# Optimization experiments

Measured on AMD Instinct MI355X. Metric: run time of the kernel, lower is better.

## Reference

```python
import jax, jax.numpy as jnp
import numpy as np

ROPE_BASE = 100.0


def _rope1d(tok, pos):
    # tok: [B, H, N, d], pos: [B, N] int. Matches croco apply_rope1d.
    d = tok.shape[-1]
    inv_freq = 1.0 / (ROPE_BASE ** (jnp.arange(0, d, 2, dtype=jnp.float32) / d))  # [d/2]
    ang = pos[:, None, :, None].astype(jnp.float32) * inv_freq  # [B,1,N,d/2]
    ang = jnp.concatenate([ang, ang], axis=-1)  # [B,1,N,d]
    cos, sin = jnp.cos(ang).astype(tok.dtype), jnp.sin(ang).astype(tok.dtype)
    x1, x2 = tok[..., : d // 2], tok[..., d // 2 :]
    rot = jnp.concatenate([-x2, x1], axis=-1)  # rotate_half
    return tok * cos + rot * sin


def _rope2d(tok, pos):
    # tok: [B, H, N, D]; first half of D uses pos[...,0] (y), second half pos[...,1] (x)
    y, x = jnp.split(tok, 2, axis=-1)
    return jnp.concatenate([_rope1d(y, pos[..., 0]), _rope1d(x, pos[..., 1])], axis=-1)


def setup_inputs() -> dict:
    key = jax.random.key(0)
    ks = jax.random.split(key, 10)
    B, N, C = 8, 1024, 768
    s = 0.02
    return {
        "query": jax.random.normal(ks[0], (B, N, C), jnp.float32),
        "key": jax.random.normal(ks[1], (B, N, C), jnp.float32),
        "value": jax.random.normal(ks[2], (B, N, C), jnp.float32),
        "qpos": jax.random.randint(ks[3], (B, N, 2), 0, 32, jnp.int32),
        "kpos": jax.random.randint(ks[4], (B, N, 2), 0, 32, jnp.int32),
        "Wq": jax.random.normal(ks[5], (C, C), jnp.float32) * s,
        "Wk": jax.random.normal(ks[6], (C, C), jnp.float32) * s,
        "Wv": jax.random.normal(ks[7], (C, C), jnp.float32) * s,
        "Wo": jax.random.normal(ks[8], (C, C), jnp.float32) * s,
        "bo": jnp.zeros((C,), jnp.float32),
    }


def reference(query, key, value, qpos, kpos, Wq, Wk, Wv, Wo, bo):
    B, Nq, C = query.shape
    H = 12
    hd = C // H
    scale = hd ** -0.5
    # projections (torch Linear: x @ W^T), then split heads -> [B,H,N,hd]
    q = jnp.einsum("bnc,dc->bnd", query, Wq).reshape(B, Nq, H, hd).transpose(0, 2, 1, 3)
    k = jnp.einsum("bnc,dc->bnd", key, Wk).reshape(B, -1, H, hd).transpose(0, 2, 1, 3)
    v = jnp.einsum("bnc,dc->bnd", value, Wv).reshape(B, -1, H, hd).transpose(0, 2, 1, 3)
    q = _rope2d(q, qpos)
    k = _rope2d(k, kpos)
    attn = jnp.einsum("bhqd,bhkd->bhqk", q, k) * scale
    attn = jax.nn.softmax(attn, axis=-1)
    x = jnp.einsum("bhqk,bhkd->bhqd", attn, v)
    x = x.transpose(0, 2, 1, 3).reshape(B, Nq, C)
    return jnp.einsum("bnc,dc->bnd", x, Wo) + bo
```

## Files before the change

kernel.cpp:

```cpp
#include <hip/hip_runtime.h>
#include <hip/hip_bf16.h>
#include <hip/hip_fp16.h>

#define B_DIM 8
#define N_DIM 1024
#define C_DIM 768
#define H_DIM 12
#define HD    64
#define M_DIM (B_DIM * N_DIM)
#define BH    (B_DIM * H_DIM)

static constexpr size_t TEN = (size_t)M_DIM * C_DIM;
static constexpr size_t WN  = (size_t)C_DIM * C_DIM;

typedef __attribute__((ext_vector_type(8))) short    s16x8;
typedef __attribute__((ext_vector_type(8))) _Float16 f16x8;
typedef __attribute__((ext_vector_type(4))) float    f32x4;

__device__ __forceinline__ unsigned short f2h(float f) {
    __half h = __float2half(f);
    return __half_as_ushort(h);
}


__global__ __launch_bounds__(256)
void convX(const float* __restrict__ q, const float* __restrict__ k,
           const float* __restrict__ v, unsigned short* __restrict__ XS)
{
    const int t  = blockIdx.z;
    const int p  = blockIdx.y;
    const int kb = blockIdx.x;
    const float* src = (t == 0) ? q : (t == 1 ? k : v);
    unsigned short* dst = XS + (size_t)t * TEN;

    const int mr = threadIdx.x & 127;
    const int gh = threadIdx.x >> 7;
    const float* s = src + ((size_t)(p * 128 + mr)) * C_DIM + kb * 32 + gh * 16;
    float4 v0 = *(const float4*)(s);
    float4 v1 = *(const float4*)(s + 4);
    float4 v2 = *(const float4*)(s + 8);
    float4 v3 = *(const float4*)(s + 12);
    float f[16] = {v0.x,v0.y,v0.z,v0.w, v1.x,v1.y,v1.z,v1.w,
                   v2.x,v2.y,v2.z,v2.w, v3.x,v3.y,v3.z,v3.w};
    #pragma unroll
    for (int gj = 0; gj < 2; ++gj) {
        int gg = gh * 2 + gj;
        s16x8 h8;
        #pragma unroll
        for (int e = 0; e < 8; ++e)
            h8[e] = (short)f2h(f[gj * 8 + e]);
        size_t a = ((((size_t)p * 24 + kb) * 4 + gg) * 128 + mr) * 8;
        *(s16x8*)(dst + a) = h8;
    }
}

__global__ __launch_bounds__(256)
void convW(const float* __restrict__ wq, const float* __restrict__ wk,
           const float* __restrict__ wv, const float* __restrict__ wo,
           unsigned short* __restrict__ WS)
{
    const int t  = blockIdx.z;
    const int p  = blockIdx.y;
    const int kb = blockIdx.x;
    const float* src = (t == 0) ? wq : (t == 1 ? wk : (t == 2 ? wv : wo));
    unsigned short* dst = WS + (size_t)t * WN;

    const int mr = threadIdx.x & 127;
    const int gh = threadIdx.x >> 7;
    const float* s = src + ((size_t)(p * 128 + mr)) * C_DIM + kb * 32 + gh * 16;
    float4 v0 = *(const float4*)(s);
    float4 v1 = *(const float4*)(s + 4);
    float4 v2 = *(const float4*)(s + 8);
    float4 v3 = *(const float4*)(s + 12);
    float f[16] = {v0.x,v0.y,v0.z,v0.w, v1.x,v1.y,v1.z,v1.w,
                   v2.x,v2.y,v2.z,v2.w, v3.x,v3.y,v3.z,v3.w};
    #pragma unroll
    for (int gj = 0; gj < 2; ++gj) {
        int gg = gh * 2 + gj;
        s16x8 h8;
        #pragma unroll
        for (int e = 0; e < 8; ++e)
            h8[e] = (short)f2h(f[gj * 8 + e]);
        size_t a = ((((size_t)p * 24 + kb) * 4 + gg) * 128 + mr) * 8;
        *(s16x8*)(dst + a) = h8;
    }
}

__global__ void angles512(float2* __restrict__ tab)
{
    int t = threadIdx.x;
    int pos = t >> 4, j = t & 15;
    float ang = (float)pos * exp2f(-(float)j * 0.41524101186092029f);
    float s, c;
    sincosf(ang, &s, &c);
    tab[t] = make_float2(c, s);
}

template<int MODE>
__global__ __launch_bounds__(256)
void gemmF(const unsigned short* __restrict__ XQ, const unsigned short* __restrict__ XK,
           const unsigned short* __restrict__ XV,
           const unsigned short* __restrict__ WQ, const unsigned short* __restrict__ WK,
           const unsigned short* __restrict__ WV,
           const int* __restrict__ qpos, const int* __restrict__ kpos,
           const float2* __restrict__ tab,
           unsigned short* __restrict__ OQ, unsigned short* __restrict__ OK_,
           unsigned short* __restrict__ OV,
           const float* __restrict__ bias, float* __restrict__ Of)
{
    __shared__ unsigned short sA[2][4][128][8];
    __shared__ unsigned short sB[2][4][128][8];

    const int tid  = threadIdx.x;
    const int lane = tid & 63;
    const int w    = tid >> 6;
    const int wr   = w >> 1, wc = w & 1;
    const int c    = lane & 15, g = lane >> 4;

    const int chunk = gridDim.x >> 3;
    const int wgid  = (blockIdx.x & 7) * chunk + (blockIdx.x >> 3);
    int z, m0, n0;
    if (MODE == 1) {
        z = wgid / 384;
        int r = wgid - z * 384;
        m0 = (r / 6) * 128;
        n0 = (r % 6) * 128;
    } else {
        z = 0;
        m0 = (wgid / 6) * 128;
        n0 = (wgid % 6) * 128;
    }

    const unsigned short *Ap, *Bp;
    if (MODE == 0 || z == 0) { Ap = XQ; Bp = WQ; }
    else if (z == 1)         { Ap = XK; Bp = WK; }
    else                     { Ap = XV; Bp = WV; }

    const size_t abase0 = (size_t)(m0 >> 7) * 24 * 4096;
    const size_t bbase0 = (size_t)(n0 >> 7) * 24 * 4096;

    f32x4 acc[4][4] = {};

    auto stage = [&](int kb, int buf) {
        #pragma unroll
        for (int t = 0; t < 4; ++t) {
            int is = w * 4 + t;
            int sel = is >> 3;
            int j   = is & 7;
            int gg  = j >> 1, half = j & 1;
            const unsigned short* srcp =
                (sel ? Bp + bbase0 : Ap + abase0) + (size_t)kb * 4096
                + (size_t)gg * 1024 + (half * 64 + lane) * 8;
            unsigned short* dstp = sel ? &sB[buf][gg][half * 64][0]
                                       : &sA[buf][gg][half * 64][0];
            __builtin_amdgcn_global_load_lds(
                (const __attribute__((address_space(1))) void*)srcp,
                (__attribute__((address_space(3))) void*)dstp,
                16, 0, 0);
        }
    };

    stage(0, 0);
    stage(1, 1);

    for (int kb = 0; kb < 24; ++kb) {
        int buf = kb & 1;
        if (kb < 23) asm volatile("s_waitcnt vmcnt(4)" ::: "memory");
        else         asm volatile("s_waitcnt vmcnt(0)" ::: "memory");
        __builtin_amdgcn_sched_barrier(0);
        __builtin_amdgcn_s_barrier();
        __builtin_amdgcn_sched_barrier(0);

        f16x8 a[4], b[4];
        #pragma unroll
        for (int mi = 0; mi < 4; ++mi)
            a[mi] = *(const f16x8*)&sA[buf][g][wr * 64 + 16 * mi + c][0];
        #pragma unroll
        for (int ni = 0; ni < 4; ++ni)
            b[ni] = *(const f16x8*)&sB[buf][g][wc * 64 + 16 * ni + c][0];
        __builtin_amdgcn_s_setprio(1);
        #pragma unroll
        for (int mi = 0; mi < 4; ++mi)
            #pragma unroll
            for (int ni = 0; ni < 4; ++ni)
                acc[mi][ni] = __builtin_amdgcn_mfma_f32_16x16x32_f16(a[mi], b[ni], acc[mi][ni], 0, 0, 0);
        __builtin_amdgcn_s_setprio(0);

        __builtin_amdgcn_sched_barrier(0);
        __builtin_amdgcn_s_barrier();
        __builtin_amdgcn_sched_barrier(0);
        if (kb + 2 < 24) stage(kb + 2, buf);
    }

    if (MODE == 0) {
        #pragma unroll
        for (int ni = 0; ni < 4; ++ni) {
            int d = n0 + wc * 64 + 16 * ni + c;
            float bv = bias[d];
            #pragma unroll
            for (int mi = 0; mi < 4; ++mi)
                #pragma unroll
                for (int r = 0; r < 4; ++r) {
                    int m = m0 + wr * 64 + 16 * mi + 4 * g + r;
                    Of[(size_t)m * C_DIM + d] = acc[mi][ni][r] + bv;
                }
        }
    } else if (z == 2) {
        #pragma unroll
        for (int ni = 0; ni < 4; ++ni) {
            int d = n0 + wc * 64 + 16 * ni + c;
            #pragma unroll
            for (int mi = 0; mi < 4; ++mi)
                #pragma unroll
                for (int r = 0; r < 4; ++r) {
                    int m = m0 + wr * 64 + 16 * mi + 4 * g + r;
                    OV[(size_t)m * C_DIM + d] = f2h(acc[mi][ni][r]);
                }
        }
    } else {
        const int* P = z ? kpos : qpos;
        unsigned short* T = z ? OK_ : OQ;
        const float scale = z ? 1.0f : 0.18033688011112042f;
        const int hh = (n0 >> 6) + wc;
        #pragma unroll
        for (int mi = 0; mi < 4; ++mi)
            #pragma unroll
            for (int r = 0; r < 4; ++r) {
                int m = m0 + wr * 64 + 16 * mi + 4 * g + r;
                int b = m >> 10, n = m & 1023;
                size_t base = ((size_t)(b * H_DIM + hh) * N_DIM + n) * HD;
                #pragma unroll
                for (int bb = 0; bb < 2; ++bb) {
                    int pos = P[2 * m + bb];
                    float2 cs = tab[pos * 16 + c];
                    float x1 = acc[mi][bb * 2 + 0][r];
                    float x2 = acc[mi][bb * 2 + 1][r];
                    float r1 = (x1 * cs.x - x2 * cs.y) * scale;
                    float r2 = (x2 * cs.x + x1 * cs.y) * scale;
                    T[base + bb * 32 + c]      = f2h(r1);
                    T[base + bb * 32 + 16 + c] = f2h(r2);
                }
            }
    }
}

__global__ __launch_bounds__(256)
void vtrans(const unsigned short* __restrict__ Vf, unsigned short* __restrict__ Vt)
{
    __shared__ unsigned short T[64][72];
    const int bh = blockIdx.y;
    const int nt = blockIdx.x;
    const int tid = threadIdx.x;
    const int b = bh / H_DIM, h = bh % H_DIM;
    const size_t hb = (size_t)bh * (N_DIM * HD);

    #pragma unroll
    for (int it = 0; it < 2; ++it) {
        int f = tid + it * 256;
        int r = f >> 3;
        int c8 = (f & 7) * 8;
        s16x8 v = *(const s16x8*)(Vf + ((size_t)(b * N_DIM + nt * 64 + r)) * C_DIM + h * HD + c8);
        #pragma unroll
        for (int j = 0; j < 8; ++j)
            T[c8 + j][r] = (unsigned short)v[j];
    }
    __syncthreads();
    #pragma unroll
    for (int it = 0; it < 2; ++it) {
        int f = tid + it * 256;
        int d = f >> 3;
        int nn = (f & 7) * 8;
        *(s16x8*)(Vt + hb + (size_t)d * N_DIM + nt * 64 + nn) = *(const s16x8*)&T[d][nn];
    }
}

__global__ __launch_bounds__(256)
void attn_f16(const unsigned short* __restrict__ Qh, const unsigned short* __restrict__ Kh,
              const unsigned short* __restrict__ Vt,
              unsigned short* __restrict__ Xb)
{
    __shared__ _Float16 sK[64][72];
    __shared__ _Float16 sV[64][72];
    __shared__ _Float16 sP[4][2][16][72];

    const int tid  = threadIdx.x;
    const int lane = tid & 63;
    const int wv   = tid >> 6;
    const int c    = lane & 15;
    const int g    = lane >> 4;

    const int bid   = blockIdx.x;
    const int xcd   = bid & 7;
    const int local = bid >> 3;
    const int bh    = xcd * 12 + (local >> 3);
    const int q0    = (local & 7) * 128;
    const size_t hb = (size_t)bh * (N_DIM * HD);

    const size_t qoffA = hb + (size_t)(q0 + wv * 32 + c) * HD;
    const size_t qoffB = qoffA + (size_t)16 * HD;
    f16x8 qA0 = *(const f16x8*)(Qh + qoffA + 8 * g);
    f16x8 qA1 = *(const f16x8*)(Qh + qoffA + 32 + 8 * g);
    f16x8 qB0 = *(const f16x8*)(Qh + qoffB + 8 * g);
    f16x8 qB1 = *(const f16x8*)(Qh + qoffB + 32 + 8 * g);

    f16x8 ones;
    #pragma unroll
    for (int e = 0; e < 8; ++e) ones[e] = (_Float16)1.0f;

    f32x4 accA[4] = {}, accB[4] = {};
    f32x4 lAcc[2] = {};

    for (int kt = 0; kt < 16; ++kt) {
        __syncthreads();
        #pragma unroll
        for (int it = 0; it < 2; ++it) {
            int f = tid + it * 256;
            int row = f >> 3;
            int ch = (f & 7) * 8;
            *(s16x8*)&sK[row][ch] = *(const s16x8*)(Kh + hb + (size_t)(kt * 64 + row) * HD + ch);
            *(s16x8*)&sV[row][ch] = *(const s16x8*)(Vt + hb + (size_t)row * N_DIM + kt * 64 + ch);
        }
        __syncthreads();

        f32x4 sA[4] = {}, sB[4] = {};
        __builtin_amdgcn_s_setprio(1);
        #pragma unroll
        for (int st = 0; st < 4; ++st) {
            f16x8 a0 = *(const f16x8*)&sK[16 * st + c][8 * g];
            f16x8 a1 = *(const f16x8*)&sK[16 * st + c][32 + 8 * g];
            sA[st] = __builtin_amdgcn_mfma_f32_16x16x32_f16(a0, qA0, sA[st], 0, 0, 0);
            sA[st] = __builtin_amdgcn_mfma_f32_16x16x32_f16(a1, qA1, sA[st], 0, 0, 0);
            sB[st] = __builtin_amdgcn_mfma_f32_16x16x32_f16(a0, qB0, sB[st], 0, 0, 0);
            sB[st] = __builtin_amdgcn_mfma_f32_16x16x32_f16(a1, qB1, sB[st], 0, 0, 0);
        }
        __builtin_amdgcn_s_setprio(0);

        #pragma unroll
        for (int st = 0; st < 4; ++st) {
            float pA[4], pB[4];
            #pragma unroll
            for (int r = 0; r < 4; ++r) {
                pA[r] = __builtin_amdgcn_exp2f(sA[st][r]);
                pB[r] = __builtin_amdgcn_exp2f(sB[st][r]);
            }
            __half2 a01 = __float22half2_rn(make_float2(pA[0], pA[1]));
            __half2 a23 = __float22half2_rn(make_float2(pA[2], pA[3]));
            __half2 b01 = __float22half2_rn(make_float2(pB[0], pB[1]));
            __half2 b23 = __float22half2_rn(make_float2(pB[2], pB[3]));
            *(uint2*)&sP[wv][0][c][16 * st + 4 * g] =
                make_uint2(*(unsigned*)&a01, *(unsigned*)&a23);
            *(uint2*)&sP[wv][1][c][16 * st + 4 * g] =
                make_uint2(*(unsigned*)&b01, *(unsigned*)&b23);
        }

        __builtin_amdgcn_s_setprio(1);
        #pragma unroll
        for (int m = 0; m < 2; ++m) {
            f16x8 pbA = *(const f16x8*)&sP[wv][0][c][32 * m + 8 * g];
            f16x8 pbB = *(const f16x8*)&sP[wv][1][c][32 * m + 8 * g];
            #pragma unroll
            for (int sd = 0; sd < 4; ++sd) {
                f16x8 va = *(const f16x8*)&sV[16 * sd + c][32 * m + 8 * g];
                accA[sd] = __builtin_amdgcn_mfma_f32_16x16x32_f16(va, pbA, accA[sd], 0, 0, 0);
                accB[sd] = __builtin_amdgcn_mfma_f32_16x16x32_f16(va, pbB, accB[sd], 0, 0, 0);
            }
            lAcc[0] = __builtin_amdgcn_mfma_f32_16x16x32_f16(ones, pbA, lAcc[0], 0, 0, 0);
            lAcc[1] = __builtin_amdgcn_mfma_f32_16x16x32_f16(ones, pbB, lAcc[1], 0, 0, 0);
        }
        __builtin_amdgcn_s_setprio(0);
    }

    float invA = 1.0f / lAcc[0][0];
    float invB = 1.0f / lAcc[1][0];

    const int b = bh / H_DIM, h = bh % H_DIM;
    #pragma unroll
    for (int sub = 0; sub < 2; ++sub) {
        const f32x4* acc = sub ? accB : accA;
        float invl = sub ? invB : invA;
        const int q = q0 + wv * 32 + sub * 16 + c;
        const int m  = b * N_DIM + q;
        const int p_ = m >> 7, mr = m & 127;
        #pragma unroll
        for (int sd = 0; sd < 4; ++sd) {
            int kdim = h * 64 + 16 * sd + 4 * g;
            int kb = kdim >> 5;
            int gg = (kdim >> 3) & 3;
            int e  = kdim & 7;
            size_t a = ((((size_t)p_ * 24 + kb) * 4 + gg) * 128 + mr) * 8 + e;
            unsigned short hs[4];
            #pragma unroll
            for (int r = 0; r < 4; ++r)
                hs[r] = f2h(acc[sd][r] * invl);
            *(uint2*)(Xb + a) =
                make_uint2((unsigned)hs[0] | ((unsigned)hs[1] << 16),
                           (unsigned)hs[2] | ((unsigned)hs[3] << 16));
        }
    }
}

extern "C" void kernel_launch(void* const* d_in, const int* in_sizes, int n_in,
                              void* d_out, int out_size, void* d_ws, size_t ws_size,
                              hipStream_t stream)
{
    const float* query = (const float*)d_in[0];
    const float* key_  = (const float*)d_in[1];
    const float* value = (const float*)d_in[2];
    const int*   qpos  = (const int*)d_in[3];
    const int*   kpos  = (const int*)d_in[4];
    const float* Wq    = (const float*)d_in[5];
    const float* Wk    = (const float*)d_in[6];
    const float* Wv    = (const float*)d_in[7];
    const float* Wo    = (const float*)d_in[8];
    const float* bo    = (const float*)d_in[9];
    float* out = (float*)d_out;

    unsigned short* XS  = (unsigned short*)d_ws;
    unsigned short* WS  = XS + 3 * TEN;
    unsigned short* Qh  = WS + 4 * WN;
    unsigned short* Kh  = Qh + TEN;
    unsigned short* Vf  = Kh + TEN;
    unsigned short* Vt  = Vf + TEN;
    unsigned short* Xb  = Vt + TEN;
    float2* tab = (float2*)(Xb + TEN);

    angles512<<<1, 512, 0, stream>>>(tab);
    convX<<<dim3(24, 64, 3), 256, 0, stream>>>(query, key_, value, XS);
    convW<<<dim3(24, 6, 4), 256, 0, stream>>>(Wq, Wk, Wv, Wo, WS);

    gemmF<1><<<dim3(1152), 256, 0, stream>>>(
        XS + 0 * TEN, XS + 1 * TEN, XS + 2 * TEN,
        WS + 0 * WN, WS + 1 * WN, WS + 2 * WN,
        qpos, kpos, tab, Qh, Kh, Vf, nullptr, nullptr);

    vtrans<<<dim3(N_DIM / 64, BH), 256, 0, stream>>>(Vf, Vt);

    attn_f16<<<dim3(768), 256, 0, stream>>>(Qh, Kh, Vt, Xb);

    gemmF<0><<<dim3(384), 256, 0, stream>>>(
        Xb, nullptr, nullptr,
        WS + 3 * WN, nullptr, nullptr,
        nullptr, nullptr, nullptr, nullptr, nullptr, nullptr, bo, out);
}
```

Before: 144.7 us.

## Triple-buffer GEMM LDS staging and register-prefetch K/V tiles in attention

```diff
diff --git a/kernel.cpp b/kernel.cpp
--- a/kernel.cpp
+++ b/kernel.cpp
@@ -108,8 +108,8 @@
            unsigned short* __restrict__ OV,
            const float* __restrict__ bias, float* __restrict__ Of)
 {
-    __shared__ unsigned short sA[2][4][128][8];
-    __shared__ unsigned short sB[2][4][128][8];
+    __shared__ unsigned short sA[3][4][128][8];
+    __shared__ unsigned short sB[3][4][128][8];
 
     const int tid  = threadIdx.x;
     const int lane = tid & 63;
@@ -162,11 +162,13 @@
 
     stage(0, 0);
     stage(1, 1);
+    stage(2, 2);
 
     for (int kb = 0; kb < 24; ++kb) {
-        int buf = kb & 1;
-        if (kb < 23) asm volatile("s_waitcnt vmcnt(4)" ::: "memory");
-        else         asm volatile("s_waitcnt vmcnt(0)" ::: "memory");
+        int buf = kb % 3;
+        if (kb < 22)      asm volatile("s_waitcnt vmcnt(8)" ::: "memory");
+        else if (kb == 22) asm volatile("s_waitcnt vmcnt(4)" ::: "memory");
+        else               asm volatile("s_waitcnt vmcnt(0)" ::: "memory");
         __builtin_amdgcn_sched_barrier(0);
         __builtin_amdgcn_s_barrier();
         __builtin_amdgcn_sched_barrier(0);
@@ -189,7 +191,7 @@
         __builtin_amdgcn_sched_barrier(0);
         __builtin_amdgcn_s_barrier();
         __builtin_amdgcn_sched_barrier(0);
-        if (kb + 2 < 24) stage(kb + 2, buf);
+        if (kb + 3 < 24) stage(kb + 3, buf);
     }
 
     if (MODE == 0) {
@@ -310,17 +312,36 @@
     f32x4 accA[4] = {}, accB[4] = {};
     f32x4 lAcc[2] = {};
 
+    const int f0 = tid, f1 = tid + 256;
+    const int row0 = f0 >> 3, ch0 = (f0 & 7) * 8;
+    const int row1 = f1 >> 3, ch1 = (f1 & 7) * 8;
+    const unsigned short* Kbase = Kh + hb;
+    const unsigned short* Vbase = Vt + hb;
+
+    s16x8 rK0 = *(const s16x8*)(Kbase + (size_t)row0 * HD + ch0);
+    s16x8 rK1 = *(const s16x8*)(Kbase + (size_t)row1 * HD + ch1);
+    s16x8 rV0 = *(const s16x8*)(Vbase + (size_t)row0 * N_DIM + ch0);
+    s16x8 rV1 = *(const s16x8*)(Vbase + (size_t)row1 * N_DIM + ch1);
+
     for (int kt = 0; kt < 16; ++kt) {
-        __syncthreads();
-        #pragma unroll
-        for (int it = 0; it < 2; ++it) {
-            int f = tid + it * 256;
-            int row = f >> 3;
-            int ch = (f & 7) * 8;
-            *(s16x8*)&sK[row][ch] = *(const s16x8*)(Kh + hb + (size_t)(kt * 64 + row) * HD + ch);
-            *(s16x8*)&sV[row][ch] = *(const s16x8*)(Vt + hb + (size_t)row * N_DIM + kt * 64 + ch);
-        }
-        __syncthreads();
+        __builtin_amdgcn_s_barrier();
+
+        *(s16x8*)&sK[row0][ch0] = rK0;
+        *(s16x8*)&sK[row1][ch1] = rK1;
+        *(s16x8*)&sV[row0][ch0] = rV0;
+        *(s16x8*)&sV[row1][ch1] = rV1;
+
+        if (kt < 15) {
+            rK0 = *(const s16x8*)(Kbase + (size_t)((kt + 1) * 64 + row0) * HD + ch0);
+            rK1 = *(const s16x8*)(Kbase + (size_t)((kt + 1) * 64 + row1) * HD + ch1);
+            rV0 = *(const s16x8*)(Vbase + (size_t)row0 * N_DIM + (kt + 1) * 64 + ch0);
+            rV1 = *(const s16x8*)(Vbase + (size_t)row1 * N_DIM + (kt + 1) * 64 + ch1);
+        }
+
+        asm volatile("s_waitcnt lgkmcnt(0)" ::: "memory");
+        __builtin_amdgcn_sched_barrier(0);
+        __builtin_amdgcn_s_barrier();
+        __builtin_amdgcn_sched_barrier(0);
 
         f32x4 sA[4] = {}, sB[4] = {};
         __builtin_amdgcn_s_setprio(1);
```

After: 145.9 us. Within noise of the previous version (+0.8%).
